# Performance work log

Hardware: AMD Instinct MI355X
Metric: run time of the kernel (lower is better)

## Reference

```python
import jax, jax.numpy as jnp
import numpy as np
import math

LOG2PI = math.log(2.0 * math.pi)


def _pair_sum(m1, v1, m2, v2, w):
    """sum_{i,j} w[i,j] * exp(delta_ij) for diagonal 2-D Gaussians.

    m1,v1: [K1,2] means / diagonal variances; m2,v2: [K2,2]; w: [K1,K2].
    Closed form of the torch code's 2x2 inverse/det/mm chain exploiting the
    fact that all covariances are diagonal (cov = diag((wh/2)^2)).
    """
    ci = 1.0 / v1[:, None, :]                      # [K1,1,2] = cov_inv_i diag
    cj = 1.0 / v2[None, :, :]                      # [1,K2,2] = cov_inv_j diag
    s = ci + cj                                    # [K1,K2,2] = cov_inv_ij diag
    mij = (m1[:, None, :] * ci + m2[None, :, :] * cj) / s   # combined mean
    quad = (jnp.sum(mij * mij * s, -1)
            - jnp.sum(m1 * m1 / v1, -1)[:, None]
            - jnp.sum(m2 * m2 / v2, -1)[None, :])            # [K1,K2]
    # log(det(cov_inv_ij) / (det(cov_inv_i) * det(cov_inv_j)))
    logdet = (jnp.sum(jnp.log(s), -1)
              + jnp.sum(jnp.log(v1), -1)[:, None]
              + jnp.sum(jnp.log(v2), -1)[None, :])           # [K1,K2]
    delta = 0.5 * (quad - logdet - 2.0 * LOG2PI)   # x_dim = 2
    return jnp.sum(w * jnp.exp(delta))


def _cs_div(p_m, p_v, p_a, q_m, q_v, q_a):
    pq = _pair_sum(p_m, p_v, q_m, q_v, p_a @ q_a.T)
    pp = _pair_sum(p_m, p_v, p_m, p_v, p_a @ p_a.T)
    qq = _pair_sum(q_m, q_v, q_m, q_v, q_a @ q_a.T)
    return 2.0 * jnp.log(pq) - jnp.log(pp) - jnp.log(qq)


def _forward(pred_bboxes, pred_labels, gt_bboxes, gt_labels):
    num_classes = pred_labels.shape[2] - 1
    pred_alpha = (jax.nn.sigmoid(pred_labels[:, :, -1])[:, :, None]
                  * jax.nn.softmax(pred_labels[:, :, :-1], axis=2))   # [bs,kp,C]
    gt_alpha = jax.nn.one_hot(gt_labels, num_classes, dtype=pred_alpha.dtype)
    pred_m = pred_bboxes[:, :, :2]
    pred_v = jnp.square(pred_bboxes[:, :, 2:] / 2.0)
    gt_m = gt_bboxes[:, :, :2]
    gt_v = jnp.square(gt_bboxes[:, :, 2:] / 2.0)
    per_img = jax.vmap(_cs_div)(gt_m, gt_v, gt_alpha, pred_m, pred_v, pred_alpha)
    return -jnp.sum(per_img)


def setup_inputs() -> dict:
    key = jax.random.key(0)
    k1, k2, k3, k4 = jax.random.split(key, 4)
    BS, KP, KG, NC = 32, 1000, 100, 80
    # widths/heights must be strictly positive -> uniform in [0.05, 1)
    pred_bboxes = jax.random.uniform(k1, (BS, KP, 4), jnp.float32, 0.05, 1.0)
    pred_labels = jax.random.normal(k2, (BS, KP, NC + 1), jnp.float32)
    gt_bboxes = jax.random.uniform(k3, (BS, KG, 4), jnp.float32, 0.05, 1.0)
    gt_labels = jax.random.randint(k4, (BS, KG), 0, NC)
    return {"pred_bboxes": pred_bboxes, "pred_labels": pred_labels,
            "gt_bboxes": gt_bboxes, "gt_labels": gt_labels}


def reference(pred_bboxes, pred_labels, gt_bboxes, gt_labels):
    return _forward(pred_bboxes, pred_labels, gt_bboxes, gt_labels)
```

## Files before the change

kernel.cpp:

```cpp
#include <hip/hip_runtime.h>
#include <math.h>

#define BS 32
#define KP 1000
#define KPP 1024
#define KG 100
#define NC 80
#define SK 96
#define LP 104
#define NT 8
#define NPAIR 36
#define NBLK (BS * NPAIR)

using bf16x8 = __attribute__((ext_vector_type(8))) short;
using f32x4  = __attribute__((ext_vector_type(4))) float;

__device__ __forceinline__ float wave_reduce_sum(float v) {
#pragma unroll
    for (int m = 32; m > 0; m >>= 1) v += __shfl_xor(v, m, 64);
    return v;
}
__device__ __forceinline__ float wave_reduce_max(float v) {
#pragma unroll
    for (int m = 32; m > 0; m >>= 1) v = fmaxf(v, __shfl_xor(v, m, 64));
    return v;
}

__device__ __forceinline__ unsigned short f2bf(float f) {
    unsigned int u = __float_as_uint(f);
    u += 0x7fffu + ((u >> 16) & 1u);
    return (unsigned short)(u >> 16);
}
__device__ __forceinline__ float bf2f(unsigned short h) {
    return __uint_as_float(((unsigned int)h) << 16);
}

__device__ __forceinline__ float kval(float4 a, float4 b) {
    float Sx = a.z + b.z, Sy = a.w + b.w;
    float dx = a.x - b.x, dy = a.y - b.y;
    float P  = Sx * Sy;
    float r  = __builtin_amdgcn_rcpf(P);
    float rs = __builtin_amdgcn_rsqf(P);
    float num = dx * dx * Sy + dy * dy * Sx;
    float q = num * r;
    return 0.15915494309189535f * rs * __expf(-0.5f * q);
}

__global__ __launch_bounds__(256) void alpha_kernel(const float* __restrict__ pl,
                                                    unsigned short* __restrict__ ah,
                                                    float* __restrict__ acc) {
    if (blockIdx.x == 0 && threadIdx.x < 128) acc[threadIdx.x] = 0.0f;
    int wave = threadIdx.x >> 6;
    int lane = threadIdx.x & 63;
    int rr = blockIdx.x * 4 + wave;
    int b = rr >> 10, r = rr & (KPP - 1);
    unsigned short* oh = ah + (size_t)rr * SK;
    if (r < KP) {
        const float* x = pl + ((size_t)b * KP + r) * (NC + 1);
        float l0 = x[lane];
        float l1 = (lane < 16) ? x[64 + lane] : -1e30f;
        float obj = x[NC];
        float m = wave_reduce_max(fmaxf(l0, l1));
        float e0 = __expf(l0 - m);
        float e1 = (lane < 16) ? __expf(l1 - m) : 0.0f;
        float s = wave_reduce_sum(e0 + e1);
        float sig = 1.0f / (1.0f + __expf(-obj));
        float sc = sig / s;
        oh[lane] = f2bf(e0 * sc);
        if (lane < 32) oh[64 + lane] = (lane < 16) ? f2bf(e1 * sc) : 0;
    } else {
        oh[lane] = 0;
        if (lane < 32) oh[64 + lane] = 0;
    }
}

__global__ __launch_bounds__(256) void ppq_kernel(const float* __restrict__ pb,
                                                  const unsigned short* __restrict__ ah,
                                                  const float* __restrict__ gtb,
                                                  const int* __restrict__ gtl,
                                                  float* __restrict__ acc_pq,
                                                  float* __restrict__ acc_pp) {
    __shared__ float4 gm[KG];
    __shared__ int gl[KG];
    __shared__ float red[4];
    int b = blockIdx.y;
    int tid = threadIdx.x;
    if (tid < KG) {
        float4 x = ((const float4*)gtb)[b * KG + tid];
        gm[tid] = make_float4(x.x, x.y, 0.25f * x.z * x.z, 0.25f * x.w * x.w);
        gl[tid] = gtl[b * KG + tid];
    }
    __syncthreads();
    float part = 0.0f;
    if (blockIdx.x < 4) {
        int j = blockIdx.x * 256 + tid;
        if (j < KP) {
            float4 x = ((const float4*)pb)[b * KP + j];
            float4 pm = make_float4(x.x, x.y, 0.25f * x.z * x.z, 0.25f * x.w * x.w);
            const unsigned short* rh = ah + ((size_t)(b << 10) + j) * SK;
#pragma unroll 4
            for (int i = 0; i < KG; ++i) {
                part += bf2f(rh[gl[i]]) * kval(gm[i], pm);
            }
        }
    } else {
        for (int p = tid; p < KG * KG; p += 256) {
            int i = p / KG;
            int j = p - i * KG;
            if (gl[i] == gl[j]) part += kval(gm[i], gm[j]);
        }
    }
    part = wave_reduce_sum(part);
    int lane = tid & 63, w = tid >> 6;
    if (lane == 0) red[w] = part;
    __syncthreads();
    if (tid == 0) {
        float s = red[0] + red[1] + red[2] + red[3];
        if (blockIdx.x < 4) atomicAdd(&acc_pq[b], s);
        else acc_pp[b] = s;
    }
}

__global__ __launch_bounds__(256, 3) void qq_kernel(const float* __restrict__ pb,
                                                    const unsigned short* __restrict__ ahg,
                                                    float* __restrict__ acc,
                                                    float* __restrict__ out) {
    __shared__ short la[128 * LP];
    __shared__ short lbb[128 * LP];
    __shared__ float red[4];
    __shared__ int last;

    int bi = blockIdx.x;
    int b = bi & 31;
    int t = bi >> 5;
    int it = 0, rem = t;
    while (rem >= NT - it) { rem -= NT - it; ++it; }
    int jt = it + rem;
    int i0 = it * 128, j0 = jt * 128;

    int tid = threadIdx.x;

    {
        int side = tid >> 7, r = tid & 127;
        int gi = (side ? j0 : i0) + r;
        float4 v = make_float4(0.0f, 0.0f, 1.0f, 1.0f);
        if (gi < KP) {
            float4 x = ((const float4*)pb)[b * KP + gi];
            v = make_float4(x.x, x.y, 0.25f * x.z * x.z, 0.25f * x.w * x.w);
        }
        short* L = side ? lbb : la;
        *(float4*)(L + r * LP + 96) = v;
    }

    {
        const float4* sa = (const float4*)(ahg + ((size_t)(b << 10) + i0) * SK);
#pragma unroll
        for (int k = 0; k < 6; ++k) {
            int o = tid + k * 256;
            int row = o / 12, slot = o - row * 12;
            *(float4*)(la + row * LP + slot * 8) = sa[o];
        }
        if (jt != it) {
            const float4* sb = (const float4*)(ahg + ((size_t)(b << 10) + j0) * SK);
#pragma unroll
            for (int k = 0; k < 6; ++k) {
                int o = tid + k * 256;
                int row = o / 12, slot = o - row * 12;
                *(float4*)(lbb + row * LP + slot * 8) = sb[o];
            }
        }
    }
    __syncthreads();
    const short* LB = (jt != it) ? lbb : la;

    int lane = tid & 63, w = tid >> 6;
    int wy = w >> 1, wx = w & 1;
    int m15 = lane & 15, quad = lane >> 4;
    int ar = wy * 64 + m15;
    int br = wx * 64 + m15;

    f32x4 c4[4][4];
#pragma unroll
    for (int r = 0; r < 4; ++r)
#pragma unroll
        for (int s = 0; s < 4; ++s) c4[r][s] = (f32x4){0.0f, 0.0f, 0.0f, 0.0f};

#pragma unroll
    for (int ks = 0; ks < 3; ++ks) {
        int kk = ks * 32 + quad * 8;
        bf16x8 bh[4];
#pragma unroll
        for (int cg = 0; cg < 4; ++cg)
            bh[cg] = *(const bf16x8*)(LB + (br + cg * 16) * LP + kk);
#pragma unroll
        for (int rg = 0; rg < 4; ++rg) {
            bf16x8 xh = *(const bf16x8*)(la + (ar + rg * 16) * LP + kk);
#pragma unroll
            for (int cg = 0; cg < 4; ++cg)
                c4[rg][cg] = __builtin_amdgcn_mfma_f32_16x16x32_bf16(xh, bh[cg], c4[rg][cg], 0, 0, 0);
        }
    }

    float4 pj[4];
    int jb = wx * 64 + m15;
#pragma unroll
    for (int cg = 0; cg < 4; ++cg)
        pj[cg] = *(const float4*)(lbb + (jb + cg * 16) * LP + 96);
    float part = 0.0f;
    int ib = wy * 64 + quad * 4;
#pragma unroll
    for (int rg = 0; rg < 4; ++rg) {
#pragma unroll
        for (int e = 0; e < 4; ++e) {
            float4 pi = *(const float4*)(la + (ib + rg * 16 + e) * LP + 96);
#pragma unroll
            for (int cg = 0; cg < 4; ++cg)
                part += c4[rg][cg][e] * kval(pi, pj[cg]);
        }
    }
    if (jt != it) part *= 2.0f;

    part = wave_reduce_sum(part);
    if (lane == 0) red[w] = part;
    __syncthreads();
    if (tid == 0) {
        atomicAdd(&acc[64 + b], red[0] + red[1] + red[2] + red[3]);
        __threadfence();
        unsigned int o = atomicAdd((unsigned int*)(acc + 96), 1u);
        last = (o == NBLK - 1) ? 1 : 0;
    }
    __syncthreads();
    if (last && tid < 64) {
        float v = 0.0f;
        if (tid < BS) {
            float pq = atomicAdd(&acc[tid], 0.0f);
            float pp = atomicAdd(&acc[32 + tid], 0.0f);
            float qq = atomicAdd(&acc[64 + tid], 0.0f);
            v = 2.0f * logf(pq) - logf(pp) - logf(qq);
        }
        v = wave_reduce_sum(v);
        if (tid == 0) out[0] = -v;
    }
}

extern "C" void kernel_launch(void* const* d_in, const int* in_sizes, int n_in,
                              void* d_out, int out_size, void* d_ws, size_t ws_size,
                              hipStream_t stream) {
    (void)in_sizes; (void)n_in; (void)out_size; (void)ws_size;
    const float* pred_bb  = (const float*)d_in[0];
    const float* pred_lab = (const float*)d_in[1];
    const float* gt_bb    = (const float*)d_in[2];
    const int*   gt_lab   = (const int*)d_in[3];
    float* out = (float*)d_out;

    unsigned short* ah = (unsigned short*)d_ws;
    float* acc = (float*)(ah + (size_t)BS * KPP * SK);
    float* acc_pq = acc;
    float* acc_pp = acc + 32;

    hipLaunchKernelGGL(alpha_kernel, dim3(BS * KPP / 4), dim3(256), 0, stream,
                       pred_lab, ah, acc);
    hipLaunchKernelGGL(ppq_kernel, dim3(5, BS), dim3(256), 0, stream,
                       pred_bb, ah, gt_bb, gt_lab, acc_pq, acc_pp);
    hipLaunchKernelGGL(qq_kernel, dim3(NBLK), dim3(256), 0, stream,
                       pred_bb, ah, acc, out);
}
```

Baseline: 116.9 us.

## Merge pq/pp and qq kernels into one launch and simplify kval

Combines the ppq and qq kernels into a single main_kernel launch. The first 160 blocks handle the pq/pp sums and the rest handle the qq MFMA tiles, and the last-block finalization now counts all blocks. This removes one kernel launch and the serialization between the two kernels, letting the cheap ppq work overlap with the qq work. It also rewrites kval with 2-wide vector ops and replaces the separate rcp with rsq squared, which saves one transcendental per pair at a small precision cost. The pp accumulation now uses atomicAdd instead of a plain store, which relies on acc being zeroed by alpha_kernel.

```diff
diff --git a/kernel.cpp b/kernel.cpp
--- a/kernel.cpp
+++ b/kernel.cpp
@@ -10,10 +10,13 @@
 #define LP 104
 #define NT 8
 #define NPAIR 36
-#define NBLK (BS * NPAIR)
+#define NQQ (BS * NPAIR)
+#define NPPQ (5 * BS)
+#define NALL (NQQ + NPPQ)
 
 using bf16x8 = __attribute__((ext_vector_type(8))) short;
 using f32x4  = __attribute__((ext_vector_type(4))) float;
+using f32x2  = __attribute__((ext_vector_type(2))) float;
 
 __device__ __forceinline__ float wave_reduce_sum(float v) {
 #pragma unroll
@@ -36,13 +39,14 @@
 }
 
 __device__ __forceinline__ float kval(float4 a, float4 b) {
-    float Sx = a.z + b.z, Sy = a.w + b.w;
-    float dx = a.x - b.x, dy = a.y - b.y;
-    float P  = Sx * Sy;
-    float r  = __builtin_amdgcn_rcpf(P);
+    f32x2 S = (f32x2){a.z, a.w} + (f32x2){b.z, b.w};
+    f32x2 d = (f32x2){a.x, a.y} - (f32x2){b.x, b.y};
+    f32x2 d2 = d * d;
+    f32x2 t = d2 * S.yx;
+    float num = t.x + t.y;
+    float P = S.x * S.y;
     float rs = __builtin_amdgcn_rsqf(P);
-    float num = dx * dx * Sy + dy * dy * Sx;
-    float q = num * r;
+    float q = num * rs * rs;
     return 0.15915494309189535f * rs * __expf(-0.5f * q);
 }
 
@@ -74,160 +78,157 @@
     }
 }
 
-__global__ __launch_bounds__(256) void ppq_kernel(const float* __restrict__ pb,
-                                                  const unsigned short* __restrict__ ah,
-                                                  const float* __restrict__ gtb,
-                                                  const int* __restrict__ gtl,
-                                                  float* __restrict__ acc_pq,
-                                                  float* __restrict__ acc_pp) {
-    __shared__ float4 gm[KG];
-    __shared__ int gl[KG];
-    __shared__ float red[4];
-    int b = blockIdx.y;
-    int tid = threadIdx.x;
-    if (tid < KG) {
-        float4 x = ((const float4*)gtb)[b * KG + tid];
-        gm[tid] = make_float4(x.x, x.y, 0.25f * x.z * x.z, 0.25f * x.w * x.w);
-        gl[tid] = gtl[b * KG + tid];
-    }
-    __syncthreads();
-    float part = 0.0f;
-    if (blockIdx.x < 4) {
-        int j = blockIdx.x * 256 + tid;
-        if (j < KP) {
-            float4 x = ((const float4*)pb)[b * KP + j];
-            float4 pm = make_float4(x.x, x.y, 0.25f * x.z * x.z, 0.25f * x.w * x.w);
-            const unsigned short* rh = ah + ((size_t)(b << 10) + j) * SK;
-#pragma unroll 4
-            for (int i = 0; i < KG; ++i) {
-                part += bf2f(rh[gl[i]]) * kval(gm[i], pm);
-            }
-        }
-    } else {
-        for (int p = tid; p < KG * KG; p += 256) {
-            int i = p / KG;
-            int j = p - i * KG;
-            if (gl[i] == gl[j]) part += kval(gm[i], gm[j]);
-        }
-    }
-    part = wave_reduce_sum(part);
-    int lane = tid & 63, w = tid >> 6;
-    if (lane == 0) red[w] = part;
-    __syncthreads();
-    if (tid == 0) {
-        float s = red[0] + red[1] + red[2] + red[3];
-        if (blockIdx.x < 4) atomicAdd(&acc_pq[b], s);
-        else acc_pp[b] = s;
-    }
-}
-
-__global__ __launch_bounds__(256, 3) void qq_kernel(const float* __restrict__ pb,
-                                                    const unsigned short* __restrict__ ahg,
-                                                    float* __restrict__ acc,
-                                                    float* __restrict__ out) {
+__global__ __launch_bounds__(256, 3) void main_kernel(const float* __restrict__ pb,
+                                                      const unsigned short* __restrict__ ahg,
+                                                      const float* __restrict__ gtb,
+                                                      const int* __restrict__ gtl,
+                                                      float* __restrict__ acc,
+                                                      float* __restrict__ out) {
     __shared__ short la[128 * LP];
     __shared__ short lbb[128 * LP];
     __shared__ float red[4];
     __shared__ int last;
 
+    int tid = threadIdx.x;
+    int lane = tid & 63, w = tid >> 6;
     int bi = blockIdx.x;
-    int b = bi & 31;
-    int t = bi >> 5;
-    int it = 0, rem = t;
-    while (rem >= NT - it) { rem -= NT - it; ++it; }
-    int jt = it + rem;
-    int i0 = it * 128, j0 = jt * 128;
-
-    int tid = threadIdx.x;
-
-    {
-        int side = tid >> 7, r = tid & 127;
-        int gi = (side ? j0 : i0) + r;
-        float4 v = make_float4(0.0f, 0.0f, 1.0f, 1.0f);
-        if (gi < KP) {
-            float4 x = ((const float4*)pb)[b * KP + gi];
-            v = make_float4(x.x, x.y, 0.25f * x.z * x.z, 0.25f * x.w * x.w);
-        }
-        short* L = side ? lbb : la;
-        *(float4*)(L + r * LP + 96) = v;
-    }
-
-    {
-        const float4* sa = (const float4*)(ahg + ((size_t)(b << 10) + i0) * SK);
-#pragma unroll
-        for (int k = 0; k < 6; ++k) {
-            int o = tid + k * 256;
-            int row = o / 12, slot = o - row * 12;
-            *(float4*)(la + row * LP + slot * 8) = sa[o];
-        }
-        if (jt != it) {
-            const float4* sb = (const float4*)(ahg + ((size_t)(b << 10) + j0) * SK);
+
+    if (bi < NPPQ) {
+        int b = bi & 31;
+        int p5 = bi >> 5;
+        float4* gm = (float4*)lbb;
+        int* gl = (int*)la;
+        if (tid < KG) {
+            float4 x = ((const float4*)gtb)[b * KG + tid];
+            gm[tid] = make_float4(x.x, x.y, 0.25f * x.z * x.z, 0.25f * x.w * x.w);
+            gl[tid] = gtl[b * KG + tid];
+        }
+        __syncthreads();
+        float part = 0.0f;
+        if (p5 < 4) {
+            int j = p5 * 256 + tid;
+            if (j < KP) {
+                float4 x = ((const float4*)pb)[b * KP + j];
+                float4 pm = make_float4(x.x, x.y, 0.25f * x.z * x.z, 0.25f * x.w * x.w);
+                const unsigned short* rh = ahg + ((size_t)(b << 10) + j) * SK;
+#pragma unroll 4
+                for (int i = 0; i < KG; ++i) {
+                    part += bf2f(rh[gl[i]]) * kval(gm[i], pm);
+                }
+            }
+        } else {
+            for (int p = tid; p < KG * KG; p += 256) {
+                int i = p / KG;
+                int j = p - i * KG;
+                if (gl[i] == gl[j]) part += kval(gm[i], gm[j]);
+            }
+        }
+        part = wave_reduce_sum(part);
+        if (lane == 0) red[w] = part;
+        __syncthreads();
+        if (tid == 0) {
+            float s = red[0] + red[1] + red[2] + red[3];
+            atomicAdd((p5 < 4) ? &acc[b] : &acc[32 + b], s);
+        }
+    } else {
+        int qi = bi - NPPQ;
+        int b = qi & 31;
+        int t = qi >> 5;
+        int it = 0, rem = t;
+        while (rem >= NT - it) { rem -= NT - it; ++it; }
+        int jt = it + rem;
+        int i0 = it * 128, j0 = jt * 128;
+
+        {
+            int side = tid >> 7, r = tid & 127;
+            int gi = (side ? j0 : i0) + r;
+            float4 v = make_float4(0.0f, 0.0f, 1.0f, 1.0f);
+            if (gi < KP) {
+                float4 x = ((const float4*)pb)[b * KP + gi];
+                v = make_float4(x.x, x.y, 0.25f * x.z * x.z, 0.25f * x.w * x.w);
+            }
+            short* L = side ? lbb : la;
+            *(float4*)(L + r * LP + 96) = v;
+        }
+
+        {
+            const float4* sa = (const float4*)(ahg + ((size_t)(b << 10) + i0) * SK);
 #pragma unroll
             for (int k = 0; k < 6; ++k) {
                 int o = tid + k * 256;
                 int row = o / 12, slot = o - row * 12;
-                *(float4*)(lbb + row * LP + slot * 8) = sb[o];
-            }
-        }
-    }
-    __syncthreads();
-    const short* LB = (jt != it) ? lbb : la;
-
-    int lane = tid & 63, w = tid >> 6;
-    int wy = w >> 1, wx = w & 1;
-    int m15 = lane & 15, quad = lane >> 4;
-    int ar = wy * 64 + m15;
-    int br = wx * 64 + m15;
-
-    f32x4 c4[4][4];
-#pragma unroll
-    for (int r = 0; r < 4; ++r)
-#pragma unroll
-        for (int s = 0; s < 4; ++s) c4[r][s] = (f32x4){0.0f, 0.0f, 0.0f, 0.0f};
-
-#pragma unroll
-    for (int ks = 0; ks < 3; ++ks) {
-        int kk = ks * 32 + quad * 8;
-        bf16x8 bh[4];
+                *(float4*)(la + row * LP + slot * 8) = sa[o];
+            }
+            if (jt != it) {
+                const float4* sb = (const float4*)(ahg + ((size_t)(b << 10) + j0) * SK);
+#pragma unroll
+                for (int k = 0; k < 6; ++k) {
+                    int o = tid + k * 256;
+                    int row = o / 12, slot = o - row * 12;
+                    *(float4*)(lbb + row * LP + slot * 8) = sb[o];
+                }
+            }
+        }
+        __syncthreads();
+        const short* LB = (jt != it) ? lbb : la;
+
+        int wy = w >> 1, wx = w & 1;
+        int m15 = lane & 15, quad = lane >> 4;
+        int ar = wy * 64 + m15;
+        int br = wx * 64 + m15;
+
+        f32x4 c4[4][4];
+#pragma unroll
+        for (int r = 0; r < 4; ++r)
+#pragma unroll
+            for (int s = 0; s < 4; ++s) c4[r][s] = (f32x4){0.0f, 0.0f, 0.0f, 0.0f};
+
+#pragma unroll
+        for (int ks = 0; ks < 3; ++ks) {
+            int kk = ks * 32 + quad * 8;
+            bf16x8 bh[4];
+#pragma unroll
+            for (int cg = 0; cg < 4; ++cg)
+                bh[cg] = *(const bf16x8*)(LB + (br + cg * 16) * LP + kk);
+#pragma unroll
+            for (int rg = 0; rg < 4; ++rg) {
+                bf16x8 xh = *(const bf16x8*)(la + (ar + rg * 16) * LP + kk);
+#pragma unroll
+                for (int cg = 0; cg < 4; ++cg)
+                    c4[rg][cg] = __builtin_amdgcn_mfma_f32_16x16x32_bf16(xh, bh[cg], c4[rg][cg], 0, 0, 0);
+            }
+        }
+
+        float4 pj[4];
+        int jb = wx * 64 + m15;
 #pragma unroll
         for (int cg = 0; cg < 4; ++cg)
-            bh[cg] = *(const bf16x8*)(LB + (br + cg * 16) * LP + kk);
+            pj[cg] = *(const float4*)(lbb + (jb + cg * 16) * LP + 96);
+        float part = 0.0f;
+        int ib = wy * 64 + quad * 4;
 #pragma unroll
         for (int rg = 0; rg < 4; ++rg) {
-            bf16x8 xh = *(const bf16x8*)(la + (ar + rg * 16) * LP + kk);
-#pragma unroll
-            for (int cg = 0; cg < 4; ++cg)
-                c4[rg][cg] = __builtin_amdgcn_mfma_f32_16x16x32_bf16(xh, bh[cg], c4[rg][cg], 0, 0, 0);
-        }
-    }
-
-    float4 pj[4];
-    int jb = wx * 64 + m15;
-#pragma unroll
-    for (int cg = 0; cg < 4; ++cg)
-        pj[cg] = *(const float4*)(lbb + (jb + cg * 16) * LP + 96);
-    float part = 0.0f;
-    int ib = wy * 64 + quad * 4;
-#pragma unroll
-    for (int rg = 0; rg < 4; ++rg) {
-#pragma unroll
-        for (int e = 0; e < 4; ++e) {
-            float4 pi = *(const float4*)(la + (ib + rg * 16 + e) * LP + 96);
-#pragma unroll
-            for (int cg = 0; cg < 4; ++cg)
-                part += c4[rg][cg][e] * kval(pi, pj[cg]);
-        }
-    }
-    if (jt != it) part *= 2.0f;
-
-    part = wave_reduce_sum(part);
-    if (lane == 0) red[w] = part;
-    __syncthreads();
+#pragma unroll
+            for (int e = 0; e < 4; ++e) {
+                float4 pi = *(const float4*)(la + (ib + rg * 16 + e) * LP + 96);
+#pragma unroll
+                for (int cg = 0; cg < 4; ++cg)
+                    part += c4[rg][cg][e] * kval(pi, pj[cg]);
+            }
+        }
+        if (jt != it) part *= 2.0f;
+
+        part = wave_reduce_sum(part);
+        if (lane == 0) red[w] = part;
+        __syncthreads();
+        if (tid == 0)
+            atomicAdd(&acc[64 + b], red[0] + red[1] + red[2] + red[3]);
+    }
+
     if (tid == 0) {
-        atomicAdd(&acc[64 + b], red[0] + red[1] + red[2] + red[3]);
         __threadfence();
         unsigned int o = atomicAdd((unsigned int*)(acc + 96), 1u);
-        last = (o == NBLK - 1) ? 1 : 0;
+        last = (o == NALL - 1) ? 1 : 0;
     }
     __syncthreads();
     if (last && tid < 64) {
@@ -255,13 +256,9 @@
 
     unsigned short* ah = (unsigned short*)d_ws;
     float* acc = (float*)(ah + (size_t)BS * KPP * SK);
-    float* acc_pq = acc;
-    float* acc_pp = acc + 32;
 
     hipLaunchKernelGGL(alpha_kernel, dim3(BS * KPP / 4), dim3(256), 0, stream,
                        pred_lab, ah, acc);
-    hipLaunchKernelGGL(ppq_kernel, dim3(5, BS), dim3(256), 0, stream,
-                       pred_bb, ah, gt_bb, gt_lab, acc_pq, acc_pp);
-    hipLaunchKernelGGL(qq_kernel, dim3(NBLK), dim3(256), 0, stream,
-                       pred_bb, ah, acc, out);
-}
+    hipLaunchKernelGGL(main_kernel, dim3(NALL), dim3(256), 0, stream,
+                       pred_bb, ah, gt_bb, gt_lab, acc, out);
+}
```

Measured after the change: 106.3 us. 9.1% less time.
